# Kernel tuning notes

Hardware: AMD Instinct MI355X
Metric: run time of the kernel (lower is better)

Reference implementation:

```python
import jax, jax.numpy as jnp
import numpy as np

N_USERS = 60000
N_ITEMS = 40000
N = N_USERS + N_ITEMS   # ncount
EMB = 64
NNZ = 3200000           # nnz of sparse_norm_adj (avg degree 32)
LN_EPS = 1e-5


def setup_inputs() -> dict:
    key = jax.random.key(0)
    ks = jax.random.split(key, 12)
    ego = jax.random.normal(ks[0], (N, EMB), jnp.float32) * 0.1
    rows = jax.random.randint(ks[1], (NNZ,), 0, N)
    cols = jax.random.randint(ks[2], (NNZ,), 0, N)
    # normalized adjacency values (non-trainable buffer)
    vals = jax.random.uniform(ks[3], (NNZ,), jnp.float32) * 0.01
    # xavier-uniform-ish scale for [64,64]: sqrt(2/(64+64)) = 0.125
    w_uu = jax.random.normal(ks[4], (EMB, EMB), jnp.float32) * 0.125
    filt_uu = jax.random.uniform(ks[5], (N_USERS,), jnp.float32, 0.99, 1.01)
    par_uu = jax.random.uniform(ks[6], (2,), jnp.float32, 0.0, 0.99)
    w_ii = jax.random.normal(ks[7], (EMB, EMB), jnp.float32) * 0.125
    filt_ii = jax.random.uniform(ks[8], (N_ITEMS,), jnp.float32, 0.99, 1.01)
    par_ii = jax.random.uniform(ks[9], (2,), jnp.float32, 0.0, 0.99)
    ln_gamma = jnp.ones((EMB,), jnp.float32)
    ln_beta = jnp.zeros((EMB,), jnp.float32)
    return {"ego_embeddings": ego, "rows": rows, "cols": cols, "vals": vals,
            "w_uu": w_uu, "filt_uu": filt_uu, "par_uu": par_uu,
            "w_ii": w_ii, "filt_ii": filt_ii, "par_ii": par_ii,
            "ln_gamma": ln_gamma, "ln_beta": ln_beta}


def _spmm(rows, cols, vals, x):
    # out[rows] += vals * x[cols]  <=>  sparse_adj @ x
    return jax.ops.segment_sum(vals[:, None] * x[cols], rows, num_segments=N)


def reference(ego_embeddings, rows, cols, vals, w_uu, filt_uu, par_uu,
              w_ii, filt_ii, par_ii, ln_gamma, ln_beta):
    res = ego_embeddings
    u = ego_embeddings[:N_USERS]
    it = ego_embeddings[N_USERS:]
    # HWNN layer with K1=K2=1 collapses to par0*par1 * diag(filter) @ X @ W
    user_ego = par_uu[0] * par_uu[1] * ((filt_uu[:, None] * u) @ w_uu) + u
    item_ego = par_ii[0] * par_ii[1] * ((filt_ii[:, None] * it) @ w_ii) + it
    ego = jnp.concatenate([user_ego, item_ego], axis=0)  # [N, EMB]
    # HGCNConv (act=False): adj @ (adj.T @ ego)
    h = jax.ops.segment_sum(vals[:, None] * ego[rows], cols, num_segments=N)  # adj.T @ ego
    y = _spmm(rows, cols, vals, h)                                            # adj @ h
    # LayerNorm (eps=1e-5, affine) + residual from the ORIGINAL input
    mu = jnp.mean(y, axis=-1, keepdims=True)
    var = jnp.var(y, axis=-1, keepdims=True)
    yn = (y - mu) / jnp.sqrt(var + LN_EPS) * ln_gamma + ln_beta
    out = yn + res
    return out[:N_USERS], out[N_USERS:]
```

## Files before the change

kernel.cpp:

```cpp
#include <hip/hip_runtime.h>

#define N_USERS 60000
#define N_ITEMS 40000
#define N_TOTAL 100000
#define EMB 64
#define LN_EPS 1e-5f

#define KPS 128
#define KSH 7
#define NSUP ((N_TOTAL + KPS - 1) / KPS)
#define EPB 8192
#define BLT 1024
#define EPT (EPB / BLT)
#define TR_ROWS 32
#define XPITCH 68
#define CAP 2048
#define SPT 512

__device__ __forceinline__ float bf2f(unsigned short h)
{ return __uint_as_float(((unsigned)h) << 16); }
__device__ __forceinline__ unsigned short f2bf(float f)
{
    unsigned u = __float_as_uint(f);
    return (unsigned short)((u + 0x7FFFu + ((u >> 16) & 1u)) >> 16);
}

__global__ void transform_tile(const float* __restrict__ x,
                               const float* __restrict__ w_uu,
                               const float* __restrict__ filt_uu,
                               const float* __restrict__ par_uu,
                               const float* __restrict__ w_ii,
                               const float* __restrict__ filt_ii,
                               const float* __restrict__ par_ii,
                               unsigned short* __restrict__ out)
{
    __shared__ float Wls[EMB * EMB];
    __shared__ float xs[TR_ROWS * XPITCH];
    const int tid = threadIdx.x;
    const int r0 = blockIdx.x * TR_ROWS;
    const int itm = (r0 >= N_USERS);
    const float* W  = itm ? w_ii : w_uu;
    const float* fb = itm ? filt_ii : filt_uu;
    const int foff  = itm ? N_USERS : 0;
    const float c   = itm ? par_ii[0] * par_ii[1] : par_uu[0] * par_uu[1];

    for (int i = tid; i < EMB * EMB / 4; i += 256)
        ((float4*)Wls)[i] = ((const float4*)W)[i];
    for (int i = tid; i < TR_ROWS * 16; i += 256) {
        const float4 v = ((const float4*)x)[r0 * 16 + i];
        *(float4*)&xs[(i >> 4) * XPITCH + (i & 15) * 4] = v;
    }
    __syncthreads();

    const int lane = tid & 63;
    const int wv = tid >> 6;
    const int rg = lane >> 4;
    const int j  = lane & 15;

#pragma unroll
    for (int it = 0; it < 2; ++it) {
        const int rl = wv * 8 + it * 4 + rg;
        const int row = r0 + rl;
        float4 acc = make_float4(0.f, 0.f, 0.f, 0.f);
#pragma unroll 8
        for (int k = 0; k < EMB; ++k) {
            const float xb = xs[rl * XPITCH + k];
            const float4 w4 = *(const float4*)&Wls[k * EMB + 4 * j];
            acc.x += xb * w4.x; acc.y += xb * w4.y;
            acc.z += xb * w4.z; acc.w += xb * w4.w;
        }
        const float cf = c * fb[row - foff];
        const float4 xv = *(const float4*)&xs[rl * XPITCH + 4 * j];
        ushort4 o;
        o.x = f2bf(cf * acc.x + xv.x);
        o.y = f2bf(cf * acc.y + xv.y);
        o.z = f2bf(cf * acc.z + xv.z);
        o.w = f2bf(cf * acc.w + xv.w);
        *(ushort4*)&out[(size_t)row * EMB + 4 * j] = o;
    }
}

__global__ void hist_sup(const int* __restrict__ rows,
                         const int* __restrict__ cols,
                         int* __restrict__ cnt_r,
                         int* __restrict__ cnt_c, int nnz)
{
    __shared__ int hr[NSUP], hc[NSUP];
    const int tid = threadIdx.x;
    for (int i = tid; i < NSUP; i += 256) { hr[i] = 0; hc[i] = 0; }
    __syncthreads();
    const int nq = nnz >> 2;
    for (int q = blockIdx.x * 256 + tid; q < nq; q += gridDim.x * 256) {
        const int4 r4 = ((const int4*)rows)[q];
        const int4 c4 = ((const int4*)cols)[q];
        atomicAdd(&hr[r4.x >> KSH], 1); atomicAdd(&hc[c4.x >> KSH], 1);
        atomicAdd(&hr[r4.y >> KSH], 1); atomicAdd(&hc[c4.y >> KSH], 1);
        atomicAdd(&hr[r4.z >> KSH], 1); atomicAdd(&hc[c4.z >> KSH], 1);
        atomicAdd(&hr[r4.w >> KSH], 1); atomicAdd(&hc[c4.w >> KSH], 1);
    }
    for (int e = (nq << 2) + blockIdx.x * 256 + tid; e < nnz; e += gridDim.x * 256) {
        atomicAdd(&hr[rows[e] >> KSH], 1);
        atomicAdd(&hc[cols[e] >> KSH], 1);
    }
    __syncthreads();
    for (int i = tid; i < NSUP; i += 256) {
        if (hr[i]) atomicAdd(&cnt_r[i], hr[i]);
        if (hc[i]) atomicAdd(&cnt_c[i], hc[i]);
    }
}

__global__ void scan_sup(const int* __restrict__ cnt_c, int* __restrict__ base_c,
                         int* __restrict__ cur_c,
                         const int* __restrict__ cnt_r, int* __restrict__ base_r,
                         int* __restrict__ cur_r)
{
    const int* cnt = blockIdx.x ? cnt_r : cnt_c;
    int* base = blockIdx.x ? base_r : base_c;
    int* cur  = blockIdx.x ? cur_r  : cur_c;
    __shared__ int wsum[16];
    const int i = threadIdx.x;
    const int lane = i & 63;
    const int wv = i >> 6;
    const int v = (i < NSUP) ? cnt[i] : 0;
    int incl = v;
#pragma unroll
    for (int off = 1; off < 64; off <<= 1) {
        const int t = __shfl_up(incl, off, 64);
        if (lane >= off) incl += t;
    }
    if (lane == 63) wsum[wv] = incl;
    __syncthreads();
    if (i == 0) {
        int run = 0;
#pragma unroll
        for (int w = 0; w < 16; ++w) { const int t = wsum[w]; wsum[w] = run; run += t; }
        base[NSUP] = run;
    }
    __syncthreads();
    const int excl = wsum[wv] + incl - v;
    if (i < NSUP) { base[i] = excl; cur[i] = excl; }
}

__global__ void __launch_bounds__(BLT, 2)
build_both(const int* __restrict__ rows,
           const int* __restrict__ cols,
           const float* __restrict__ vals,
           int* __restrict__ cur_c, int2* __restrict__ pairs_c,
           int* __restrict__ cur_r, int2* __restrict__ pairs_r, int nnz)
{
    __shared__ int hist_c[NSUP];
    __shared__ int hist_r[NSUP];
    __shared__ int lcur[NSUP];

    const int tid = threadIdx.x;
    const int e0 = blockIdx.x * EPB;
    const int ecnt = min(EPB, nnz - e0);

    for (int i = tid; i < NSUP; i += BLT) { hist_c[i] = 0; hist_r[i] = 0; }
    __syncthreads();

    int myr[EPT], myc[EPT];
    float myv[EPT];
#pragma unroll
    for (int i = 0; i < EPT; ++i) {
        const int s = tid + i * BLT;
        if (s < ecnt) {
            const int e = e0 + s;
            myr[i] = rows[e]; myc[i] = cols[e]; myv[i] = vals[e];
            atomicAdd(&hist_c[myc[i] >> KSH], 1);
            atomicAdd(&hist_r[myr[i] >> KSH], 1);
        } else myr[i] = -1;
    }
    __syncthreads();

    if (tid < NSUP) {
        const int v = hist_c[tid];
        lcur[tid] = v ? atomicAdd(&cur_c[tid], v) : 0;
    }
    __syncthreads();
#pragma unroll
    for (int i = 0; i < EPT; ++i) {
        if (myr[i] >= 0) {
            const int g = myc[i] >> KSH;
            const int pos = atomicAdd(&lcur[g], 1);
            pairs_c[pos] = make_int2(myr[i] | ((myc[i] & (KPS - 1)) << 20),
                                     __float_as_int(myv[i]));
        }
    }
    __syncthreads();

    if (tid < NSUP) {
        const int v = hist_r[tid];
        lcur[tid] = v ? atomicAdd(&cur_r[tid], v) : 0;
    }
    __syncthreads();
#pragma unroll
    for (int i = 0; i < EPT; ++i) {
        if (myr[i] >= 0) {
            const int g = myr[i] >> KSH;
            const int pos = atomicAdd(&lcur[g], 1);
            pairs_r[pos] = make_int2(myc[i] | ((myr[i] & (KPS - 1)) << 20),
                                     __float_as_int(myv[i]));
        }
    }
}

template <bool LN>
__global__ void __launch_bounds__(SPT, 6)
spmm_fused(const int* __restrict__ base,
           const int2* __restrict__ pairs,
           const unsigned short* __restrict__ src,
           const float* __restrict__ ego,
           const float* __restrict__ gamma,
           const float* __restrict__ beta,
           unsigned short* __restrict__ dstb,
           float* __restrict__ dstf)
{
    __shared__ int2 stage[CAP];
    __shared__ int2 sorted[CAP];
    __shared__ int cnt[KPS];
    __shared__ int kbase[KPS];
    __shared__ int kcur[KPS];

    const int tid = threadIdx.x;
    const int sup = blockIdx.x;
    const int beg = base[sup];
    const int end = base[sup + 1];
    const int g = tid >> 4;
    const int l = tid & 15;

    float4 acc[4];
#pragma unroll
    for (int i = 0; i < 4; ++i) acc[i] = make_float4(0.f, 0.f, 0.f, 0.f);

    if (tid < KPS) cnt[tid] = 0;
    __syncthreads();

    int c0 = beg;
    int csz = min(CAP, end - c0);
    for (int i = tid; i < csz; i += SPT) {
        const int2 v = pairs[c0 + i];
        stage[i] = v;
        atomicAdd(&cnt[(v.x >> 20) & (KPS - 1)], 1);
    }
    __syncthreads();

    while (csz > 0) {
        if (tid < 64) {
            const int ca = cnt[tid * 2];
            const int cb = cnt[tid * 2 + 1];
            const int tsum = ca + cb;
            int incl = tsum;
#pragma unroll
            for (int off = 1; off < 64; off <<= 1) {
                const int t = __shfl_up(incl, off, 64);
                if (tid >= off) incl += t;
            }
            const int run = incl - tsum;
            kbase[tid * 2] = run;          kcur[tid * 2] = run;
            kbase[tid * 2 + 1] = run + ca; kcur[tid * 2 + 1] = run + ca;
            cnt[tid * 2] = 0; cnt[tid * 2 + 1] = 0;
        }
        __syncthreads();

        for (int i = tid; i < csz; i += SPT) {
            const int2 v = stage[i];
            const int pos = atomicAdd(&kcur[(v.x >> 20) & (KPS - 1)], 1);
            sorted[pos] = v;
        }
        __syncthreads();

        const int nc0 = c0 + csz;
        const int ncsz = min(CAP, end - nc0);

#pragma unroll
        for (int rr = 0; rr < 4; ++rr) {
            const int k = g * 4 + rr;
            int j = kbase[k];
            const int e = kcur[k];
            float4 a = acc[rr];
            for (; j + 8 <= e; j += 8) {
                int2 p[8]; ushort4 s[8];
#pragma unroll
                for (int u = 0; u < 8; ++u) p[u] = sorted[j + u];
#pragma unroll
                for (int u = 0; u < 8; ++u)
                    s[u] = ((const ushort4*)(src + (size_t)(p[u].x & 0x1FFFF) * EMB))[l];
#pragma unroll
                for (int u = 0; u < 8; ++u) {
                    const float v = __int_as_float(p[u].y);
                    a.x += v * bf2f(s[u].x); a.y += v * bf2f(s[u].y);
                    a.z += v * bf2f(s[u].z); a.w += v * bf2f(s[u].w);
                }
            }
            for (; j + 4 <= e; j += 4) {
                int2 p[4]; ushort4 s[4];
#pragma unroll
                for (int u = 0; u < 4; ++u) p[u] = sorted[j + u];
#pragma unroll
                for (int u = 0; u < 4; ++u)
                    s[u] = ((const ushort4*)(src + (size_t)(p[u].x & 0x1FFFF) * EMB))[l];
#pragma unroll
                for (int u = 0; u < 4; ++u) {
                    const float v = __int_as_float(p[u].y);
                    a.x += v * bf2f(s[u].x); a.y += v * bf2f(s[u].y);
                    a.z += v * bf2f(s[u].z); a.w += v * bf2f(s[u].w);
                }
            }
            for (; j < e; ++j) {
                const int2 p = sorted[j];
                const ushort4 s = ((const ushort4*)(src + (size_t)(p.x & 0x1FFFF) * EMB))[l];
                const float v = __int_as_float(p.y);
                a.x += v * bf2f(s.x); a.y += v * bf2f(s.y);
                a.z += v * bf2f(s.z); a.w += v * bf2f(s.w);
            }
            acc[rr] = a;
        }

        for (int i = tid; i < ncsz; i += SPT) {
            const int2 v = pairs[nc0 + i];
            stage[i] = v;
            atomicAdd(&cnt[(v.x >> 20) & (KPS - 1)], 1);
        }
        c0 = nc0; csz = ncsz;
        __syncthreads();
    }

    const int r0 = sup * KPS + g * 4;
    if (!LN) {
#pragma unroll
        for (int rr = 0; rr < 4; ++rr) {
            const int row = r0 + rr;
            if (row < N_TOTAL) {
                ushort4 o;
                o.x = f2bf(acc[rr].x); o.y = f2bf(acc[rr].y);
                o.z = f2bf(acc[rr].z); o.w = f2bf(acc[rr].w);
                ((ushort4*)dstb)[(size_t)row * 16 + l] = o;
            }
        }
    } else {
        const float4 gm = ((const float4*)gamma)[l];
        const float4 bt = ((const float4*)beta)[l];
#pragma unroll
        for (int rr = 0; rr < 4; ++rr) {
            const int row = r0 + rr;
            const float4 a = acc[rr];
            float s  = a.x + a.y + a.z + a.w;
            float s2 = a.x * a.x + a.y * a.y + a.z * a.z + a.w * a.w;
#pragma unroll
            for (int m = 1; m <= 8; m <<= 1) {
                s  += __shfl_xor(s,  m, 64);
                s2 += __shfl_xor(s2, m, 64);
            }
            const float mu  = s * (1.0f / EMB);
            const float var = s2 * (1.0f / EMB) - mu * mu;
            const float inv = rsqrtf(var + LN_EPS);
            if (row < N_TOTAL) {
                const float4 eg = ((const float4*)(ego + (size_t)row * EMB))[l];
                float4 o;
                o.x = (a.x - mu) * inv * gm.x + bt.x + eg.x;
                o.y = (a.y - mu) * inv * gm.y + bt.y + eg.y;
                o.z = (a.z - mu) * inv * gm.z + bt.z + eg.z;
                o.w = (a.w - mu) * inv * gm.w + bt.w + eg.w;
                ((float4*)(dstf + (size_t)row * EMB))[l] = o;
            }
        }
    }
}

__global__ void transform_kernel(const float* __restrict__ x,
                                 const float* __restrict__ W,
                                 const float* __restrict__ filt,
                                 const float* __restrict__ par,
                                 float* __restrict__ out, int nrows)
{
    __shared__ float Ws[EMB * EMB];
    const int tid = threadIdx.x;
    for (int i = tid; i < EMB * EMB; i += blockDim.x) Ws[i] = W[i];
    __syncthreads();
    const float c = par[0] * par[1];
    const int lane = tid & 63;
    const int wave = tid >> 6;
    const int r0 = blockIdx.x * 32;
    for (int rr = wave; rr < 32; rr += 4) {
        const int r = r0 + rr;
        if (r >= nrows) break;
        const float xv = x[(size_t)r * EMB + lane];
        float acc = 0.f;
#pragma unroll
        for (int k = 0; k < EMB; ++k) {
            const float xk = __shfl(xv, k, 64);
            acc += xk * Ws[k * EMB + lane];
        }
        out[(size_t)r * EMB + lane] = c * filt[r] * acc + xv;
    }
}

__global__ void spmm_scatter(const int* __restrict__ src_idx,
                             const int* __restrict__ dst_idx,
                             const float* __restrict__ vals,
                             const float* __restrict__ src,
                             float* __restrict__ dst, int nnz)
{
    const long long t = (long long)blockIdx.x * blockDim.x + threadIdx.x;
    const int e = (int)(t >> 4);
    const int l = (int)(t & 15);
    if (e >= nnz) return;
    const int s = src_idx[e];
    const int d = dst_idx[e];
    const float v = vals[e];
    const float4 xv = ((const float4*)(src + (size_t)s * EMB))[l];
    float* dp = dst + (size_t)d * EMB + l * 4;
    atomicAdd(dp + 0, v * xv.x);
    atomicAdd(dp + 1, v * xv.y);
    atomicAdd(dp + 2, v * xv.z);
    atomicAdd(dp + 3, v * xv.w);
}

__global__ void ln_residual(const float* y,
                            const float* __restrict__ ego,
                            const float* __restrict__ gamma,
                            const float* __restrict__ beta,
                            float* out, int nrows)
{
    const int lane = threadIdx.x & 63;
    const int wave = threadIdx.x >> 6;
    const int r = blockIdx.x * 4 + wave;
    if (r >= nrows) return;
    const float v = y[(size_t)r * EMB + lane];
    float s = v, s2 = v * v;
#pragma unroll
    for (int off = 32; off > 0; off >>= 1) {
        s  += __shfl_down(s,  off, 64);
        s2 += __shfl_down(s2, off, 64);
    }
    s  = __shfl(s,  0, 64);
    s2 = __shfl(s2, 0, 64);
    const float mu  = s * (1.0f / EMB);
    const float var = s2 * (1.0f / EMB) - mu * mu;
    const float inv = rsqrtf(var + LN_EPS);
    out[(size_t)r * EMB + lane] =
        (v - mu) * inv * gamma[lane] + beta[lane] + ego[(size_t)r * EMB + lane];
}

extern "C" void kernel_launch(void* const* d_in, const int* in_sizes, int n_in,
                              void* d_out, int out_size, void* d_ws, size_t ws_size,
                              hipStream_t stream)
{
    const float* ego     = (const float*)d_in[0];
    const int*   rows    = (const int*)  d_in[1];
    const int*   cols    = (const int*)  d_in[2];
    const float* vals    = (const float*)d_in[3];
    const float* w_uu    = (const float*)d_in[4];
    const float* filt_uu = (const float*)d_in[5];
    const float* par_uu  = (const float*)d_in[6];
    const float* w_ii    = (const float*)d_in[7];
    const float* filt_ii = (const float*)d_in[8];
    const float* par_ii  = (const float*)d_in[9];
    const float* gamma   = (const float*)d_in[10];
    const float* beta    = (const float*)d_in[11];
    float* out = (float*)d_out;
    const int nnz = in_sizes[1];

    const size_t emb_elems = (size_t)N_TOTAL * EMB;
    const size_t emb_bytes = emb_elems * sizeof(float);
    const size_t bf_bytes  = emb_elems * sizeof(unsigned short);

    const size_t need = 2 * bf_bytes + 2 * (size_t)nnz * sizeof(int2)
                        + (size_t)(6 * (NSUP + 1)) * sizeof(int);

    if (ws_size >= need) {
        unsigned short* ego2b = (unsigned short*)d_ws;
        unsigned short* hb    = ego2b + emb_elems;
        int2* pairs_c = (int2*)(hb + emb_elems);
        int2* pairs_r = pairs_c + nnz;
        int*  cnt_c  = (int*)(pairs_r + nnz);
        int*  cnt_r  = cnt_c + NSUP;
        int*  base_c = cnt_r + NSUP;
        int*  cur_c  = base_c + (NSUP + 1);
        int*  base_r = cur_c + NSUP;
        int*  cur_r  = base_r + (NSUP + 1);

        hipMemsetAsync(cnt_c, 0, 2 * NSUP * sizeof(int), stream);

        hist_sup<<<512, 256, 0, stream>>>(rows, cols, cnt_r, cnt_c, nnz);
        scan_sup<<<2, 1024, 0, stream>>>(cnt_c, base_c, cur_c,
                                         cnt_r, base_r, cur_r);

        transform_tile<<<N_TOTAL / TR_ROWS, 256, 0, stream>>>(
            ego, w_uu, filt_uu, par_uu, w_ii, filt_ii, par_ii, ego2b);

        const int l1b = (nnz + EPB - 1) / EPB;
        build_both<<<l1b, BLT, 0, stream>>>(rows, cols, vals,
                                            cur_c, pairs_c, cur_r, pairs_r, nnz);

        spmm_fused<false><<<NSUP, SPT, 0, stream>>>(
            base_c, pairs_c, ego2b, nullptr, nullptr, nullptr, hb, nullptr);

        spmm_fused<true><<<NSUP, SPT, 0, stream>>>(
            base_r, pairs_r, hb, ego, gamma, beta, nullptr, out);
    } else {
        float* ego2 = (float*)d_ws;
        float* h    = ego2 + emb_elems;
        hipMemsetAsync(h,   0, emb_bytes, stream);
        hipMemsetAsync(out, 0, emb_bytes, stream);

        transform_kernel<<<(N_USERS + 31) / 32, 256, 0, stream>>>(
            ego, w_uu, filt_uu, par_uu, ego2, N_USERS);
        transform_kernel<<<(N_ITEMS + 31) / 32, 256, 0, stream>>>(
            ego + (size_t)N_USERS * EMB, w_ii, filt_ii, par_ii,
            ego2 + (size_t)N_USERS * EMB, N_ITEMS);

        const long long thr = (long long)nnz * 16;
        const int sblocks = (int)((thr + 255) / 256);
        spmm_scatter<<<sblocks, 256, 0, stream>>>(rows, cols, vals, ego2, h, nnz);
        spmm_scatter<<<sblocks, 256, 0, stream>>>(cols, rows, vals, h, out, nnz);

        const int rb = (N_TOTAL + 3) / 4;
        ln_residual<<<rb, 256, 0, stream>>>(out, ego, gamma, beta, out, N_TOTAL);
    }
}
```

Before: 360.5 us.

## Widen SpMM gathers to 16-byte loads and merge CSR bucket scatter passes

In the SpMM, each row is now handled by 8 lanes that each load 8 bf16 values (uint4), instead of 16 lanes that each load 4 (ushort4). This halves the number of gather instructions per edge, and each thread now owns 2 rows instead of 4. The 8-wide unrolled inner loop is dropped, leaving 4-wide and tail loops, which may reduce memory-level parallelism per thread. Separately, the edge bucketing kernel reserves its global offsets for both the column and row orderings at once and scatters both in one pass. This removes two barriers but uses an extra shared cursor array.

Result: slower. 368.0 us (+2.1%).

```diff
diff --git a/kernel.cpp b/kernel.cpp
--- a/kernel.cpp
+++ b/kernel.cpp
@@ -24,6 +24,10 @@
     unsigned u = __float_as_uint(f);
     return (unsigned short)((u + 0x7FFFu + ((u >> 16) & 1u)) >> 16);
 }
+__device__ __forceinline__ float blo(unsigned u)
+{ return __uint_as_float(u << 16); }
+__device__ __forceinline__ float bhi(unsigned u)
+{ return __uint_as_float(u & 0xFFFF0000u); }
 
 __global__ void transform_tile(const float* __restrict__ x,
                                const float* __restrict__ w_uu,
@@ -150,7 +154,8 @@
 {
     __shared__ int hist_c[NSUP];
     __shared__ int hist_r[NSUP];
-    __shared__ int lcur[NSUP];
+    __shared__ int lcur_c[NSUP];
+    __shared__ int lcur_r[NSUP];
 
     const int tid = threadIdx.x;
     const int e0 = blockIdx.x * EPB;
@@ -174,33 +179,23 @@
     __syncthreads();
 
     if (tid < NSUP) {
-        const int v = hist_c[tid];
-        lcur[tid] = v ? atomicAdd(&cur_c[tid], v) : 0;
-    }
-    __syncthreads();
+        const int vc = hist_c[tid];
+        lcur_c[tid] = vc ? atomicAdd(&cur_c[tid], vc) : 0;
+        const int vr = hist_r[tid];
+        lcur_r[tid] = vr ? atomicAdd(&cur_r[tid], vr) : 0;
+    }
+    __syncthreads();
+
 #pragma unroll
     for (int i = 0; i < EPT; ++i) {
         if (myr[i] >= 0) {
-            const int g = myc[i] >> KSH;
-            const int pos = atomicAdd(&lcur[g], 1);
-            pairs_c[pos] = make_int2(myr[i] | ((myc[i] & (KPS - 1)) << 20),
-                                     __float_as_int(myv[i]));
-        }
-    }
-    __syncthreads();
-
-    if (tid < NSUP) {
-        const int v = hist_r[tid];
-        lcur[tid] = v ? atomicAdd(&cur_r[tid], v) : 0;
-    }
-    __syncthreads();
-#pragma unroll
-    for (int i = 0; i < EPT; ++i) {
-        if (myr[i] >= 0) {
-            const int g = myr[i] >> KSH;
-            const int pos = atomicAdd(&lcur[g], 1);
-            pairs_r[pos] = make_int2(myc[i] | ((myr[i] & (KPS - 1)) << 20),
-                                     __float_as_int(myv[i]));
+            const int vv = __float_as_int(myv[i]);
+            const int gc = myc[i] >> KSH;
+            const int pc = atomicAdd(&lcur_c[gc], 1);
+            pairs_c[pc] = make_int2(myr[i] | ((myc[i] & (KPS - 1)) << 20), vv);
+            const int gr = myr[i] >> KSH;
+            const int pr = atomicAdd(&lcur_r[gr], 1);
+            pairs_r[pr] = make_int2(myc[i] | ((myr[i] & (KPS - 1)) << 20), vv);
         }
     }
 }
@@ -226,12 +221,15 @@
     const int sup = blockIdx.x;
     const int beg = base[sup];
     const int end = base[sup + 1];
-    const int g = tid >> 4;
-    const int l = tid & 15;
-
-    float4 acc[4];
-#pragma unroll
-    for (int i = 0; i < 4; ++i) acc[i] = make_float4(0.f, 0.f, 0.f, 0.f);
+    const int g = tid >> 3;
+    const int l = tid & 7;
+
+    float4 aLo[2], aHi[2];
+#pragma unroll
+    for (int i = 0; i < 2; ++i) {
+        aLo[i] = make_float4(0.f, 0.f, 0.f, 0.f);
+        aHi[i] = make_float4(0.f, 0.f, 0.f, 0.f);
+    }
 
     if (tid < KPS) cnt[tid] = 0;
     __syncthreads();
@@ -274,47 +272,37 @@
         const int ncsz = min(CAP, end - nc0);
 
 #pragma unroll
-        for (int rr = 0; rr < 4; ++rr) {
-            const int k = g * 4 + rr;
+        for (int rr = 0; rr < 2; ++rr) {
+            const int k = g * 2 + rr;
             int j = kbase[k];
             const int e = kcur[k];
-            float4 a = acc[rr];
-            for (; j + 8 <= e; j += 8) {
-                int2 p[8]; ushort4 s[8];
-#pragma unroll
-                for (int u = 0; u < 8; ++u) p[u] = sorted[j + u];
-#pragma unroll
-                for (int u = 0; u < 8; ++u)
-                    s[u] = ((const ushort4*)(src + (size_t)(p[u].x & 0x1FFFF) * EMB))[l];
-#pragma unroll
-                for (int u = 0; u < 8; ++u) {
-                    const float v = __int_as_float(p[u].y);
-                    a.x += v * bf2f(s[u].x); a.y += v * bf2f(s[u].y);
-                    a.z += v * bf2f(s[u].z); a.w += v * bf2f(s[u].w);
-                }
-            }
+            float4 lo = aLo[rr], hi = aHi[rr];
             for (; j + 4 <= e; j += 4) {
-                int2 p[4]; ushort4 s[4];
+                int2 p[4]; uint4 d[4];
 #pragma unroll
                 for (int u = 0; u < 4; ++u) p[u] = sorted[j + u];
 #pragma unroll
                 for (int u = 0; u < 4; ++u)
-                    s[u] = ((const ushort4*)(src + (size_t)(p[u].x & 0x1FFFF) * EMB))[l];
+                    d[u] = ((const uint4*)(src + (size_t)(p[u].x & 0x1FFFF) * EMB))[l];
 #pragma unroll
                 for (int u = 0; u < 4; ++u) {
                     const float v = __int_as_float(p[u].y);
-                    a.x += v * bf2f(s[u].x); a.y += v * bf2f(s[u].y);
-                    a.z += v * bf2f(s[u].z); a.w += v * bf2f(s[u].w);
+                    lo.x += v * blo(d[u].x); lo.y += v * bhi(d[u].x);
+                    lo.z += v * blo(d[u].y); lo.w += v * bhi(d[u].y);
+                    hi.x += v * blo(d[u].z); hi.y += v * bhi(d[u].z);
+                    hi.z += v * blo(d[u].w); hi.w += v * bhi(d[u].w);
                 }
             }
             for (; j < e; ++j) {
                 const int2 p = sorted[j];
-                const ushort4 s = ((const ushort4*)(src + (size_t)(p.x & 0x1FFFF) * EMB))[l];
+                const uint4 d = ((const uint4*)(src + (size_t)(p.x & 0x1FFFF) * EMB))[l];
                 const float v = __int_as_float(p.y);
-                a.x += v * bf2f(s.x); a.y += v * bf2f(s.y);
-                a.z += v * bf2f(s.z); a.w += v * bf2f(s.w);
+                lo.x += v * blo(d.x); lo.y += v * bhi(d.x);
+                lo.z += v * blo(d.y); lo.w += v * bhi(d.y);
+                hi.x += v * blo(d.z); hi.y += v * bhi(d.z);
+                hi.z += v * blo(d.w); hi.w += v * bhi(d.w);
             }
-            acc[rr] = a;
+            aLo[rr] = lo; aHi[rr] = hi;
         }
 
         for (int i = tid; i < ncsz; i += SPT) {
@@ -326,29 +314,34 @@
         __syncthreads();
     }
 
-    const int r0 = sup * KPS + g * 4;
+    const int r0 = sup * KPS + g * 2;
     if (!LN) {
 #pragma unroll
-        for (int rr = 0; rr < 4; ++rr) {
+        for (int rr = 0; rr < 2; ++rr) {
             const int row = r0 + rr;
             if (row < N_TOTAL) {
-                ushort4 o;
-                o.x = f2bf(acc[rr].x); o.y = f2bf(acc[rr].y);
-                o.z = f2bf(acc[rr].z); o.w = f2bf(acc[rr].w);
-                ((ushort4*)dstb)[(size_t)row * 16 + l] = o;
+                uint4 o;
+                o.x = ((unsigned)f2bf(aLo[rr].y) << 16) | f2bf(aLo[rr].x);
+                o.y = ((unsigned)f2bf(aLo[rr].w) << 16) | f2bf(aLo[rr].z);
+                o.z = ((unsigned)f2bf(aHi[rr].y) << 16) | f2bf(aHi[rr].x);
+                o.w = ((unsigned)f2bf(aHi[rr].w) << 16) | f2bf(aHi[rr].z);
+                ((uint4*)dstb)[(size_t)row * 8 + l] = o;
             }
         }
     } else {
-        const float4 gm = ((const float4*)gamma)[l];
-        const float4 bt = ((const float4*)beta)[l];
-#pragma unroll
-        for (int rr = 0; rr < 4; ++rr) {
+        const float4 gmL = ((const float4*)gamma)[2 * l];
+        const float4 gmH = ((const float4*)gamma)[2 * l + 1];
+        const float4 btL = ((const float4*)beta)[2 * l];
+        const float4 btH = ((const float4*)beta)[2 * l + 1];
+#pragma unroll
+        for (int rr = 0; rr < 2; ++rr) {
             const int row = r0 + rr;
-            const float4 a = acc[rr];
-            float s  = a.x + a.y + a.z + a.w;
-            float s2 = a.x * a.x + a.y * a.y + a.z * a.z + a.w * a.w;
-#pragma unroll
-            for (int m = 1; m <= 8; m <<= 1) {
+            const float4 lo = aLo[rr], hi = aHi[rr];
+            float s  = lo.x + lo.y + lo.z + lo.w + hi.x + hi.y + hi.z + hi.w;
+            float s2 = lo.x * lo.x + lo.y * lo.y + lo.z * lo.z + lo.w * lo.w
+                     + hi.x * hi.x + hi.y * hi.y + hi.z * hi.z + hi.w * hi.w;
+#pragma unroll
+            for (int m = 1; m <= 4; m <<= 1) {
                 s  += __shfl_xor(s,  m, 64);
                 s2 += __shfl_xor(s2, m, 64);
             }
@@ -356,13 +349,19 @@
             const float var = s2 * (1.0f / EMB) - mu * mu;
             const float inv = rsqrtf(var + LN_EPS);
             if (row < N_TOTAL) {
-                const float4 eg = ((const float4*)(ego + (size_t)row * EMB))[l];
-                float4 o;
-                o.x = (a.x - mu) * inv * gm.x + bt.x + eg.x;
-                o.y = (a.y - mu) * inv * gm.y + bt.y + eg.y;
-                o.z = (a.z - mu) * inv * gm.z + bt.z + eg.z;
-                o.w = (a.w - mu) * inv * gm.w + bt.w + eg.w;
-                ((float4*)(dstf + (size_t)row * EMB))[l] = o;
+                const float4 egL = ((const float4*)(ego + (size_t)row * EMB))[2 * l];
+                const float4 egH = ((const float4*)(ego + (size_t)row * EMB))[2 * l + 1];
+                float4 oL, oH;
+                oL.x = (lo.x - mu) * inv * gmL.x + btL.x + egL.x;
+                oL.y = (lo.y - mu) * inv * gmL.y + btL.y + egL.y;
+                oL.z = (lo.z - mu) * inv * gmL.z + btL.z + egL.z;
+                oL.w = (lo.w - mu) * inv * gmL.w + btL.w + egL.w;
+                oH.x = (hi.x - mu) * inv * gmH.x + btH.x + egH.x;
+                oH.y = (hi.y - mu) * inv * gmH.y + btH.y + egH.y;
+                oH.z = (hi.z - mu) * inv * gmH.z + btH.z + egH.z;
+                oH.w = (hi.w - mu) * inv * gmH.w + btH.w + egH.w;
+                ((float4*)(dstf + (size_t)row * EMB))[2 * l] = oL;
+                ((float4*)(dstf + (size_t)row * EMB))[2 * l + 1] = oH;
             }
         }
     }
```
